# Performance work log

Hardware: AMD Instinct MI355X
Metric: run time of the kernel (lower is better)

Reference implementation:

```python
import jax, jax.numpy as jnp
import numpy as np

B, S, D_MODEL, H = 2, 2048, 1024, 16
DIMS = D_MODEL // H  # 64


def setup_inputs() -> dict:
    key = jax.random.key(0)
    ks = jax.random.split(key, 7)
    scale = 1.0 / np.sqrt(D_MODEL)
    x = jax.random.normal(ks[0], (B, S, D_MODEL), dtype=jnp.float32)
    # Stacked per-head projection params: nn.Linear(d_model, dims) per head
    Wq = jax.random.uniform(ks[1], (H, DIMS, D_MODEL), minval=-scale, maxval=scale, dtype=jnp.float32)
    Wk = jax.random.uniform(ks[2], (H, DIMS, D_MODEL), minval=-scale, maxval=scale, dtype=jnp.float32)
    Wv = jax.random.uniform(ks[3], (H, DIMS, D_MODEL), minval=-scale, maxval=scale, dtype=jnp.float32)
    bq = jax.random.uniform(ks[4], (H, DIMS), minval=-scale, maxval=scale, dtype=jnp.float32)
    bk = jax.random.uniform(ks[5], (H, DIMS), minval=-scale, maxval=scale, dtype=jnp.float32)
    bv = jax.random.uniform(ks[6], (H, DIMS), minval=-scale, maxval=scale, dtype=jnp.float32)
    return {"x": x, "Wq": Wq, "Wk": Wk, "Wv": Wv, "bq": bq, "bk": bk, "bv": bv}


def reference(x, Wq, Wk, Wv, bq, bk, bv):
    # Per-head linear projections: [B,S,D] x [H,E,D] -> [B,H,S,E]
    q = jnp.einsum('bsd,hed->bhse', x, Wq) + bq[None, :, None, :]
    k = jnp.einsum('bsd,hed->bhse', x, Wk) + bk[None, :, None, :]
    v = jnp.einsum('bsd,hed->bhse', x, Wv) + bv[None, :, None, :]
    norm = DIMS ** (-0.5)
    # (q @ k^T) * norm @ v  -- NO softmax, as in the source
    scores = jnp.einsum('bhse,bhte->bhst', q, k) * norm  # [B,H,S,S]
    out = jnp.einsum('bhst,bhte->bhse', scores, v)       # [B,H,S,E]
    # concat heads along feature dim (head order matches torch.cat)
    return out.transpose(0, 2, 1, 3).reshape(B, S, H * DIMS)
```

## Files before the change

kernel.cpp:

```cpp
#include <hip/hip_runtime.h>


typedef __attribute__((ext_vector_type(8))) __bf16 bf16x8;
typedef __attribute__((ext_vector_type(8))) short short8;
typedef __attribute__((ext_vector_type(4))) float f32x4;
typedef __attribute__((ext_vector_type(4))) unsigned short ushort4v;

#define NX  4194304
#define NW1 1048576
#define NW  3145728

__device__ __forceinline__ float bf2f(unsigned short u) {
  union { unsigned int i; float f; } v; v.i = ((unsigned int)u) << 16; return v.f;
}
__device__ __forceinline__ unsigned short f2bf(float f) {
  union { float f; unsigned int i; } v; v.f = f;
  unsigned int u = v.i;
  u += 0x7fffu + ((u >> 16) & 1u);
  return (unsigned short)(u >> 16);
}

__device__ __forceinline__ void gload_lds16(const void* g, void* l) {
  __builtin_amdgcn_global_load_lds(
      (const __attribute__((address_space(1))) void*)(unsigned long long)(g),
      (__attribute__((address_space(3))) void*)(unsigned int)(unsigned long long)(l),
      16, 0, 0);
}

__global__ __launch_bounds__(256) void convert_pack(
    const float* __restrict__ x,
    const float* __restrict__ wq, const float* __restrict__ wk,
    const float* __restrict__ wv,
    const float* __restrict__ bq, const float* __restrict__ bk,
    const float* __restrict__ bv,
    unsigned short* __restrict__ Xbf, unsigned short* __restrict__ Wcat,
    float* __restrict__ Bcat)
{
  const long long t8 = ((long long)blockIdx.x * 256 + threadIdx.x) * 8;
  const float* src;
  unsigned short* dst;
  long long off;
  if (t8 < NX) {
    src = x; dst = Xbf; off = t8;
  } else if (t8 < NX + NW) {
    const long long w = t8 - NX;
    const int z = (int)(w >> 20);
    off = w & (NW1 - 1);
    src = (z == 0) ? wq : (z == 1) ? wk : wv;
    dst = Wcat + (long long)z * NW1;
  } else if (t8 < NX + NW + 3072) {
    const long long bo = t8 - (NX + NW);
    const int z = (int)(bo >> 10);
    const long long o2 = bo & 1023;
    const float* bsrc = (z == 0) ? bq : (z == 1) ? bk : bv;
    *(f32x4*)(Bcat + z * 1024 + o2)     = *(const f32x4*)(bsrc + o2);
    *(f32x4*)(Bcat + z * 1024 + o2 + 4) = *(const f32x4*)(bsrc + o2 + 4);
    return;
  } else {
    return;
  }
  f32x4 v0 = *(const f32x4*)(src + off);
  f32x4 v1 = *(const f32x4*)(src + off + 4);
  union { short8 s; unsigned short u[8]; } o;
#pragma unroll
  for (int j = 0; j < 4; ++j) {
    o.u[j]     = f2bf(v0[j]);
    o.u[4 + j] = f2bf(v1[j]);
  }
  *(short8*)(dst + off) = o.s;
}

#define ABUF_B 16384
#define BBUF_B 12288
#define TILE_B 28672
__global__ __launch_bounds__(512, 2) void qkv_gemm(
    const unsigned short* __restrict__ Xbf,
    const unsigned short* __restrict__ Wcat,
    const float* __restrict__ Bcat,
    unsigned short* __restrict__ Qt,
    unsigned short* __restrict__ Kt,
    unsigned short* __restrict__ Vt)
{
  __shared__ unsigned char lds[4 * TILE_B];

  const int tid = threadIdx.x;
  int bid = blockIdx.x;
  bid = (bid & 7) * 32 + (bid >> 3);
  const int colBase = (bid & 15) * 192;
  const int rowBase = (bid >> 4) * 256;

  const int lane = tid & 63;
  const int wid  = tid >> 6;
  const int wr = (wid >> 2) * 128;
  const int wc = (wid & 3) * 48;
  const int lr = lane & 15;
  const int lk = lane >> 4;
  const int fofs = (lk ^ ((lr >> 1) & 3)) << 4;

  const bool isA = (tid < 256);
  const int tloc = isA ? tid : (tid - 256);

  const unsigned short* gptr[4];
  int lofs[4];
#pragma unroll
  for (int l = 0; l < 4; ++l) {
    const int unit = l * 256 + tloc;
    const int row  = unit >> 2;
    const int sc   = ((unit & 3) ^ ((row >> 1) & 3)) << 3;
    const int rowc = (!isA && row > 191) ? 0 : row;
    gptr[l] = isA ? (Xbf  + (size_t)(rowBase + rowc) * 1024 + sc)
                  : (Wcat + (size_t)(colBase + rowc) * 1024 + sc);
    lofs[l] = (isA ? 0 : ABUF_B) + unit * 16;
  }

  f32x4 acc[8][3] = {};

#define STAGE(j3)                                                    \
  { unsigned char* Sb_ = lds + ((j3) & 3) * TILE_B;                  \
    const int ko_ = (j3) * 32;                                       \
    if (isA) {                                                       \
      _Pragma("unroll") for (int l = 0; l < 4; ++l)                  \
        gload_lds16(gptr[l] + ko_, Sb_ + lofs[l]);                   \
    } else {                                                         \
      _Pragma("unroll") for (int l = 0; l < 3; ++l)                  \
        gload_lds16(gptr[l] + ko_, Sb_ + lofs[l]);                   \
    } }

#define KSTEP(j, DOSTAGE, VMA, VMB)                                       \
  { if (isA) asm volatile("s_waitcnt vmcnt(" #VMA ")" ::: "memory");      \
    else     asm volatile("s_waitcnt vmcnt(" #VMB ")" ::: "memory");      \
    asm volatile("s_barrier" ::: "memory");                               \
    const unsigned char* Ab_ = lds + ((j) & 3) * TILE_B;                  \
    const unsigned char* Bb_ = Ab_ + ABUF_B;                              \
    bf16x8 a_[8], b_[3];                                                  \
    _Pragma("unroll") for (int m = 0; m < 8; ++m)                         \
      a_[m] = *(const bf16x8*)(Ab_ + (wr + m * 16 + lr) * 64 + fofs);     \
    _Pragma("unroll") for (int n = 0; n < 3; ++n)                         \
      b_[n] = *(const bf16x8*)(Bb_ + (wc + n * 16 + lr) * 64 + fofs);     \
    if (DOSTAGE) STAGE((j) + 3);                                          \
    __builtin_amdgcn_s_setprio(1);                                        \
    _Pragma("unroll") for (int m = 0; m < 8; ++m)                         \
      _Pragma("unroll") for (int n = 0; n < 3; ++n)                       \
        acc[m][n] = __builtin_amdgcn_mfma_f32_16x16x32_bf16(              \
            a_[m], b_[n], acc[m][n], 0, 0, 0);                            \
    __builtin_amdgcn_s_setprio(0);                                        \
  }

  STAGE(0); STAGE(1); STAGE(2);

  for (int j = 0; j < 29; ++j) KSTEP(j, true, 8, 6);
  KSTEP(29, false, 8, 6);
  KSTEP(30, false, 4, 3);
  KSTEP(31, false, 0, 0);
#undef KSTEP
#undef STAGE

  const int bB = rowBase >> 11;
#pragma unroll
  for (int n = 0; n < 3; ++n) {
    const int colG = colBase + wc + n * 16 + lr;
    const float bval = Bcat[colG];
    const int zone = colG >> 10;
    unsigned short* __restrict__ T = (zone == 0) ? Qt : (zone == 1) ? Kt : Vt;
    const int hf = (colG >> 6) & 15;
    const int f  = colG & 63;
    const size_t rowOff = ((size_t)(bB * 16 + hf) * 64 + f) * 2048;
#pragma unroll
    for (int m = 0; m < 8; ++m) {
      const int t = (rowBase + wr + m * 16 + lk * 4) & 2047;
      ushort4v pk;
#pragma unroll
      for (int jj = 0; jj < 4; ++jj)
        pk[jj] = f2bf(acc[m][n][jj] + bval);
      *(ushort4v*)&T[rowOff + t] = pk;
    }
  }
}

__global__ __launch_bounds__(64) void kv_outer(
    const unsigned short* __restrict__ Kt,
    const unsigned short* __restrict__ Vt,
    float* __restrict__ Mpart)
{
  const int lane = threadIdx.x;
  const int blk = blockIdx.x;
  const int bh = blk >> 3, tc = blk & 7;
  const int lr = lane & 15, lk = lane >> 4;
  const size_t base = (size_t)bh * 64 * 2048;

  f32x4 acc[4][4] = {};
#pragma unroll
  for (int ks = 0; ks < 8; ++ks) {
    const int t0 = tc * 256 + ks * 32 + lk * 8;
    bf16x8 af[4], bf[4];
#pragma unroll
    for (int m = 0; m < 4; ++m)
      af[m] = *(const bf16x8*)&Kt[base + (size_t)(m * 16 + lr) * 2048 + t0];
#pragma unroll
    for (int n = 0; n < 4; ++n)
      bf[n] = *(const bf16x8*)&Vt[base + (size_t)(n * 16 + lr) * 2048 + t0];
#pragma unroll
    for (int m = 0; m < 4; ++m)
#pragma unroll
      for (int n = 0; n < 4; ++n)
        acc[m][n] = __builtin_amdgcn_mfma_f32_16x16x32_bf16(af[m], bf[n], acc[m][n], 0, 0, 0);
  }
  float* out = Mpart + (size_t)blk * 4096;
#pragma unroll
  for (int m = 0; m < 4; ++m)
#pragma unroll
    for (int n = 0; n < 4; ++n)
#pragma unroll
      for (int j = 0; j < 4; ++j)
        out[(m * 16 + lk * 4 + j) * 64 + n * 16 + lr] = acc[m][n][j];
}

__global__ __launch_bounds__(256) void qm_out(
    const unsigned short* __restrict__ Qt, const float* __restrict__ Mpart,
    float* __restrict__ Out)
{
  __shared__ float Ms[64 * 64];
  __shared__ float Qst[64 * 132];
  const int tid = threadIdx.x;
  const int b = blockIdx.z, h = blockIdx.y, s0 = blockIdx.x * 128;
  const int bh = b * 16 + h;

#pragma unroll
  for (int i = 0; i < 4; ++i) {
    const int off = i * 1024 + tid * 4;
    f32x4 s = {};
#pragma unroll
    for (int ch = 0; ch < 8; ++ch)
      s += *(const f32x4*)&Mpart[((size_t)bh * 8 + ch) * 4096 + off];
    s *= 0.125f;
    *(f32x4*)&Ms[off] = s;
  }
  const size_t qbase = (size_t)bh * 64 * 2048;
#pragma unroll
  for (int i = 0; i < 4; ++i) {
    const int slot = i * 256 + tid;
    const int f = slot >> 4, c = slot & 15;
    short8 q = *(const short8*)&Qt[qbase + (size_t)f * 2048 + s0 + c * 8];
#pragma unroll
    for (int j = 0; j < 8; ++j)
      Qst[f * 132 + c * 8 + j] = bf2f((unsigned short)q[j]);
  }
  __syncthreads();

  const int s = (tid >> 3) * 4;
  const int e0 = (tid & 7) * 8;
  float acc2[4][8] = {};
  for (int f = 0; f < 64; ++f) {
    f32x4 m0 = *(const f32x4*)&Ms[f * 64 + e0];
    f32x4 m1 = *(const f32x4*)&Ms[f * 64 + e0 + 4];
#pragma unroll
    for (int i = 0; i < 4; ++i) {
      const float q = Qst[f * 132 + s + i];
#pragma unroll
      for (int j = 0; j < 4; ++j) {
        acc2[i][j]     += q * m0[j];
        acc2[i][j + 4] += q * m1[j];
      }
    }
  }
  const size_t obase = ((size_t)b * 2048 + s0) * 1024 + h * 64;
#pragma unroll
  for (int i = 0; i < 4; ++i) {
    f32x4 o0 = { acc2[i][0], acc2[i][1], acc2[i][2], acc2[i][3] };
    f32x4 o1 = { acc2[i][4], acc2[i][5], acc2[i][6], acc2[i][7] };
    *(f32x4*)&Out[obase + (size_t)(s + i) * 1024 + e0]     = o0;
    *(f32x4*)&Out[obase + (size_t)(s + i) * 1024 + e0 + 4] = o1;
  }
}

extern "C" void kernel_launch(void* const* d_in, const int* in_sizes, int n_in,
                              void* d_out, int out_size, void* d_ws, size_t ws_size,
                              hipStream_t stream) {
  const float* x  = (const float*)d_in[0];
  const float* Wq = (const float*)d_in[1];
  const float* Wk = (const float*)d_in[2];
  const float* Wv = (const float*)d_in[3];
  const float* bq = (const float*)d_in[4];
  const float* bk = (const float*)d_in[5];
  const float* bv = (const float*)d_in[6];
  float* out = (float*)d_out;

  char* ws = (char*)d_ws;
  const size_t MiB = 1024ull * 1024ull;
  unsigned short* Xbf   = (unsigned short*)(ws);
  unsigned short* Wcat  = (unsigned short*)(ws + 8  * MiB);
  float*          Bcat  = (float*)         (ws + 14 * MiB);
  unsigned short* Qt    = (unsigned short*)(ws + 15 * MiB);
  unsigned short* Kt    = (unsigned short*)(ws + 23 * MiB);
  unsigned short* Vt    = (unsigned short*)(ws + 31 * MiB);
  float*          Mpart = (float*)         (ws + 39 * MiB);

  convert_pack<<<3586, 256, 0, stream>>>(x, Wq, Wk, Wv, bq, bk, bv,
                                         Xbf, Wcat, Bcat);
  qkv_gemm<<<256, 512, 0, stream>>>(Xbf, Wcat, Bcat, Qt, Kt, Vt);
  kv_outer<<<256, 64, 0, stream>>>(Kt, Vt, Mpart);
  qm_out<<<dim3(16, 16, 2), 256, 0, stream>>>(Qt, Mpart, out);
}
```

Baseline: 66.50 us.

## Replace direct global-to-LDS loads with register-staged software pipeline in QKV GEMM

The QKV projection GEMM no longer uses global_load_lds DMA into a 4-deep LDS ring. Each thread now prefetches three k-steps of tiles into registers and writes the next tile into a 3-deep LDS ring while the current one is consumed by MFMAs. The LDS footprint drops by one tile, and the explicit vmcnt waits give way to compiler-managed waits plus lgkmcnt waits. The cost is many extra VGPRs for the staging buffers, which may hurt occupancy under launch_bounds(512,2), and the added LDS write instructions.

```diff
diff --git a/kernel.cpp b/kernel.cpp
--- a/kernel.cpp
+++ b/kernel.cpp
@@ -18,13 +18,6 @@
   unsigned int u = v.i;
   u += 0x7fffu + ((u >> 16) & 1u);
   return (unsigned short)(u >> 16);
-}
-
-__device__ __forceinline__ void gload_lds16(const void* g, void* l) {
-  __builtin_amdgcn_global_load_lds(
-      (const __attribute__((address_space(1))) void*)(unsigned long long)(g),
-      (__attribute__((address_space(3))) void*)(unsigned int)(unsigned long long)(l),
-      16, 0, 0);
 }
 
 __global__ __launch_bounds__(256) void convert_pack(
@@ -71,7 +64,6 @@
 }
 
 #define ABUF_B 16384
-#define BBUF_B 12288
 #define TILE_B 28672
 __global__ __launch_bounds__(512, 2) void qkv_gemm(
     const unsigned short* __restrict__ Xbf,
@@ -81,7 +73,7 @@
     unsigned short* __restrict__ Kt,
     unsigned short* __restrict__ Vt)
 {
-  __shared__ unsigned char lds[4 * TILE_B];
+  __shared__ unsigned char lds[3 * TILE_B];
 
   const int tid = threadIdx.x;
   int bid = blockIdx.x;
@@ -98,9 +90,10 @@
   const int fofs = (lk ^ ((lr >> 1) & 3)) << 4;
 
   const bool isA = (tid < 256);
-  const int tloc = isA ? tid : (tid - 256);
-
-  const unsigned short* gptr[4];
+  const int nload = isA ? 4 : 3;
+  const int tloc = tid & 255;
+
+  const unsigned short* gp[4];
   int lofs[4];
 #pragma unroll
   for (int l = 0; l < 4; ++l) {
@@ -108,52 +101,59 @@
     const int row  = unit >> 2;
     const int sc   = ((unit & 3) ^ ((row >> 1) & 3)) << 3;
     const int rowc = (!isA && row > 191) ? 0 : row;
-    gptr[l] = isA ? (Xbf  + (size_t)(rowBase + rowc) * 1024 + sc)
-                  : (Wcat + (size_t)(colBase + rowc) * 1024 + sc);
+    gp[l]  = isA ? (Xbf  + (size_t)(rowBase + rowc) * 1024 + sc)
+                 : (Wcat + (size_t)(colBase + rowc) * 1024 + sc);
     lofs[l] = (isA ? 0 : ABUF_B) + unit * 16;
   }
 
   f32x4 acc[8][3] = {};
-
-#define STAGE(j3)                                                    \
-  { unsigned char* Sb_ = lds + ((j3) & 3) * TILE_B;                  \
-    const int ko_ = (j3) * 32;                                       \
-    if (isA) {                                                       \
-      _Pragma("unroll") for (int l = 0; l < 4; ++l)                  \
-        gload_lds16(gptr[l] + ko_, Sb_ + lofs[l]);                   \
-    } else {                                                         \
-      _Pragma("unroll") for (int l = 0; l < 3; ++l)                  \
-        gload_lds16(gptr[l] + ko_, Sb_ + lofs[l]);                   \
-    } }
-
-#define KSTEP(j, DOSTAGE, VMA, VMB)                                       \
-  { if (isA) asm volatile("s_waitcnt vmcnt(" #VMA ")" ::: "memory");      \
-    else     asm volatile("s_waitcnt vmcnt(" #VMB ")" ::: "memory");      \
-    asm volatile("s_barrier" ::: "memory");                               \
-    const unsigned char* Ab_ = lds + ((j) & 3) * TILE_B;                  \
-    const unsigned char* Bb_ = Ab_ + ABUF_B;                              \
-    bf16x8 a_[8], b_[3];                                                  \
-    _Pragma("unroll") for (int m = 0; m < 8; ++m)                         \
-      a_[m] = *(const bf16x8*)(Ab_ + (wr + m * 16 + lr) * 64 + fofs);     \
-    _Pragma("unroll") for (int n = 0; n < 3; ++n)                         \
-      b_[n] = *(const bf16x8*)(Bb_ + (wc + n * 16 + lr) * 64 + fofs);     \
-    if (DOSTAGE) STAGE((j) + 3);                                          \
-    __builtin_amdgcn_s_setprio(1);                                        \
-    _Pragma("unroll") for (int m = 0; m < 8; ++m)                         \
-      _Pragma("unroll") for (int n = 0; n < 3; ++n)                       \
-        acc[m][n] = __builtin_amdgcn_mfma_f32_16x16x32_bf16(              \
-            a_[m], b_[n], acc[m][n], 0, 0, 0);                            \
-    __builtin_amdgcn_s_setprio(0);                                        \
-  }
-
-  STAGE(0); STAGE(1); STAGE(2);
-
-  for (int j = 0; j < 29; ++j) KSTEP(j, true, 8, 6);
-  KSTEP(29, false, 8, 6);
-  KSTEP(30, false, 4, 3);
-  KSTEP(31, false, 0, 0);
-#undef KSTEP
-#undef STAGE
+  short8 stg[3][4];
+
+#pragma unroll
+  for (int s = 0; s < 3; ++s)
+#pragma unroll
+    for (int l = 0; l < 4; ++l)
+      if (l < nload) stg[s][l] = *(const short8*)(gp[l] + s * 32);
+#pragma unroll
+  for (int l = 0; l < 4; ++l)
+    if (l < nload) *(short8*)(lds + lofs[l]) = stg[0][l];
+  asm volatile("s_waitcnt lgkmcnt(0)" ::: "memory");
+
+#define ITER(J, U, U1)                                                     \
+  if ((J) < 32) {                                                          \
+    __builtin_amdgcn_s_barrier();                                          \
+    __builtin_amdgcn_sched_barrier(0);                                     \
+    const unsigned char* Ab_ = lds + (U) * TILE_B;                         \
+    const unsigned char* Bb_ = Ab_ + ABUF_B;                               \
+    bf16x8 a_[8], b_[3];                                                   \
+    _Pragma("unroll") for (int m = 0; m < 8; ++m)                          \
+      a_[m] = *(const bf16x8*)(Ab_ + (wr + m * 16 + lr) * 64 + fofs);      \
+    _Pragma("unroll") for (int n = 0; n < 3; ++n)                          \
+      b_[n] = *(const bf16x8*)(Bb_ + (wc + n * 16 + lr) * 64 + fofs);      \
+    if ((J) + 1 < 32) {                                                    \
+      unsigned char* Wb_ = lds + (U1) * TILE_B;                            \
+      _Pragma("unroll") for (int l = 0; l < 4; ++l)                        \
+        if (l < nload) *(short8*)(Wb_ + lofs[l]) = stg[U1][l];             \
+    }                                                                      \
+    if ((J) + 3 < 32) {                                                    \
+      _Pragma("unroll") for (int l = 0; l < 4; ++l)                        \
+        if (l < nload) stg[U][l] = *(const short8*)(gp[l] + ((J) + 3) * 32);\
+    }                                                                      \
+    __builtin_amdgcn_s_setprio(1);                                         \
+    _Pragma("unroll") for (int m = 0; m < 8; ++m)                          \
+      _Pragma("unroll") for (int n = 0; n < 3; ++n)                        \
+        acc[m][n] = __builtin_amdgcn_mfma_f32_16x16x32_bf16(               \
+            a_[m], b_[n], acc[m][n], 0, 0, 0);                             \
+    __builtin_amdgcn_s_setprio(0);                                         \
+    asm volatile("s_waitcnt lgkmcnt(0)" ::: "memory");                     \
+  }
+
+  for (int jb = 0; jb < 32; jb += 3) {
+    ITER(jb + 0, 0, 1);
+    ITER(jb + 1, 1, 2);
+    ITER(jb + 2, 2, 0);
+  }
+#undef ITER
 
   const int bB = rowBase >> 11;
 #pragma unroll
```

Measured after the change: 67.05 us. About the same (+0.8%).

## Restructure QKV GEMM to 256x256 tiles with BK=64 double-buffered LDS

Applied to the files above, without the earlier changes.

The QKV projection GEMM now uses 256x256 output tiles (192 blocks, one block per CU) instead of 256x192 tiles (256 blocks). Each iteration loads a 64-wide K slice into one of two 64KB LDS buffers, and staging of the next slice is interleaved between the two MFMA sub-steps. The LDS XOR swizzle is dropped. The goal is more reuse per loaded byte, fewer blocks so the grid fits in one wave on 256 CUs, and fewer barriers. The trade-offs are lower occupancy (launch bounds 1), more accumulator registers, possible LDS bank conflicts now that the swizzle is gone, and 64 idle CUs.

```diff
diff --git a/kernel.cpp b/kernel.cpp
--- a/kernel.cpp
+++ b/kernel.cpp
@@ -70,10 +70,7 @@
   *(short8*)(dst + off) = o.s;
 }
 
-#define ABUF_B 16384
-#define BBUF_B 12288
-#define TILE_B 28672
-__global__ __launch_bounds__(512, 2) void qkv_gemm(
+__global__ __launch_bounds__(512, 1) void qkv_gemm(
     const unsigned short* __restrict__ Xbf,
     const unsigned short* __restrict__ Wcat,
     const float* __restrict__ Bcat,
@@ -81,83 +78,166 @@
     unsigned short* __restrict__ Kt,
     unsigned short* __restrict__ Vt)
 {
-  __shared__ unsigned char lds[4 * TILE_B];
+  __shared__ unsigned char lds[131072];
 
   const int tid = threadIdx.x;
   int bid = blockIdx.x;
-  bid = (bid & 7) * 32 + (bid >> 3);
-  const int colBase = (bid & 15) * 192;
-  const int rowBase = (bid >> 4) * 256;
+  bid = (bid & 7) * 24 + (bid >> 3);
+  const int colBase = (bid % 12) * 256;
+  const int rowBase = (bid / 12) * 256;
 
   const int lane = tid & 63;
   const int wid  = tid >> 6;
   const int wr = (wid >> 2) * 128;
-  const int wc = (wid & 3) * 48;
+  const int wc = (wid & 3) * 64;
   const int lr = lane & 15;
   const int lk = lane >> 4;
-  const int fofs = (lk ^ ((lr >> 1) & 3)) << 4;
-
-  const bool isA = (tid < 256);
-  const int tloc = isA ? tid : (tid - 256);
-
-  const unsigned short* gptr[4];
-  int lofs[4];
-#pragma unroll
-  for (int l = 0; l < 4; ++l) {
-    const int unit = l * 256 + tloc;
-    const int row  = unit >> 2;
-    const int sc   = ((unit & 3) ^ ((row >> 1) & 3)) << 3;
-    const int rowc = (!isA && row > 191) ? 0 : row;
-    gptr[l] = isA ? (Xbf  + (size_t)(rowBase + rowc) * 1024 + sc)
-                  : (Wcat + (size_t)(colBase + rowc) * 1024 + sc);
-    lofs[l] = (isA ? 0 : ABUF_B) + unit * 16;
-  }
-
-  f32x4 acc[8][3] = {};
-
-#define STAGE(j3)                                                    \
-  { unsigned char* Sb_ = lds + ((j3) & 3) * TILE_B;                  \
-    const int ko_ = (j3) * 32;                                       \
-    if (isA) {                                                       \
-      _Pragma("unroll") for (int l = 0; l < 4; ++l)                  \
-        gload_lds16(gptr[l] + ko_, Sb_ + lofs[l]);                   \
-    } else {                                                         \
-      _Pragma("unroll") for (int l = 0; l < 3; ++l)                  \
-        gload_lds16(gptr[l] + ko_, Sb_ + lofs[l]);                   \
-    } }
-
-#define KSTEP(j, DOSTAGE, VMA, VMB)                                       \
-  { if (isA) asm volatile("s_waitcnt vmcnt(" #VMA ")" ::: "memory");      \
-    else     asm volatile("s_waitcnt vmcnt(" #VMB ")" ::: "memory");      \
-    asm volatile("s_barrier" ::: "memory");                               \
-    const unsigned char* Ab_ = lds + ((j) & 3) * TILE_B;                  \
-    const unsigned char* Bb_ = Ab_ + ABUF_B;                              \
-    bf16x8 a_[8], b_[3];                                                  \
-    _Pragma("unroll") for (int m = 0; m < 8; ++m)                         \
-      a_[m] = *(const bf16x8*)(Ab_ + (wr + m * 16 + lr) * 64 + fofs);     \
-    _Pragma("unroll") for (int n = 0; n < 3; ++n)                         \
-      b_[n] = *(const bf16x8*)(Bb_ + (wc + n * 16 + lr) * 64 + fofs);     \
-    if (DOSTAGE) STAGE((j) + 3);                                          \
-    __builtin_amdgcn_s_setprio(1);                                        \
-    _Pragma("unroll") for (int m = 0; m < 8; ++m)                         \
-      _Pragma("unroll") for (int n = 0; n < 3; ++n)                       \
-        acc[m][n] = __builtin_amdgcn_mfma_f32_16x16x32_bf16(              \
-            a_[m], b_[n], acc[m][n], 0, 0, 0);                            \
-    __builtin_amdgcn_s_setprio(0);                                        \
-  }
-
-  STAGE(0); STAGE(1); STAGE(2);
-
-  for (int j = 0; j < 29; ++j) KSTEP(j, true, 8, 6);
-  KSTEP(29, false, 8, 6);
-  KSTEP(30, false, 4, 3);
-  KSTEP(31, false, 0, 0);
-#undef KSTEP
-#undef STAGE
+
+  const size_t aoff = (size_t)(rowBase + (tid >> 2)) * 1024 + (tid & 3) * 8;
+  const size_t boff = (size_t)(colBase + (tid >> 2)) * 1024 + (tid & 3) * 8;
+  const int d1 = tid * 16, d2 = 8192 + tid * 16;
+
+#define STG(secl, gsrc)                                   \
+  { gload_lds16((gsrc),               (secl) + d1);       \
+    gload_lds16((gsrc) + 128 * 1024,  (secl) + d2); }
+
+  f32x4 acc[8][4] = {};
+
+  STG(lds + 0,     Xbf  + aoff + 0);
+  STG(lds + 32768, Wcat + boff + 0);
+  STG(lds + 16384, Xbf  + aoff + 32);
+  STG(lds + 49152, Wcat + boff + 32);
+
+  const int frA = (wr + lr) * 64 + lk * 16;
+  const int frB = (wc + lr) * 64 + lk * 16;
+
+  for (int t = 0; t < 16; ++t) {
+    const unsigned char* bufc = lds + (t & 1) * 65536;
+    unsigned char* bufn = lds + ((t + 1) & 1) * 65536;
+    const size_t kno = (size_t)(t + 1) * 64;
+    const bool st = (t < 15);
+
+    bf16x8 a0, a1, a2, a3, a4, a5, a6, a7, b0, b1;
+
+    asm volatile("s_waitcnt vmcnt(4)" ::: "memory");
+    __builtin_amdgcn_s_barrier();
+    {
+      const unsigned char* As = bufc;
+      const unsigned char* Bs = bufc + 32768;
+      a0 = *(const bf16x8*)(As + frA);
+      a1 = *(const bf16x8*)(As + frA + 1024);
+      a2 = *(const bf16x8*)(As + frA + 2048);
+      a3 = *(const bf16x8*)(As + frA + 3072);
+      a4 = *(const bf16x8*)(As + frA + 4096);
+      a5 = *(const bf16x8*)(As + frA + 5120);
+      a6 = *(const bf16x8*)(As + frA + 6144);
+      a7 = *(const bf16x8*)(As + frA + 7168);
+      b0 = *(const bf16x8*)(Bs + frB);
+      b1 = *(const bf16x8*)(Bs + frB + 1024);
+      if (st) STG(bufn + 0, Xbf + aoff + kno);
+      __builtin_amdgcn_s_setprio(1);
+      acc[0][0] = __builtin_amdgcn_mfma_f32_16x16x32_bf16(a0, b0, acc[0][0], 0, 0, 0);
+      acc[1][0] = __builtin_amdgcn_mfma_f32_16x16x32_bf16(a1, b0, acc[1][0], 0, 0, 0);
+      acc[2][0] = __builtin_amdgcn_mfma_f32_16x16x32_bf16(a2, b0, acc[2][0], 0, 0, 0);
+      acc[3][0] = __builtin_amdgcn_mfma_f32_16x16x32_bf16(a3, b0, acc[3][0], 0, 0, 0);
+      acc[4][0] = __builtin_amdgcn_mfma_f32_16x16x32_bf16(a4, b0, acc[4][0], 0, 0, 0);
+      acc[5][0] = __builtin_amdgcn_mfma_f32_16x16x32_bf16(a5, b0, acc[5][0], 0, 0, 0);
+      acc[6][0] = __builtin_amdgcn_mfma_f32_16x16x32_bf16(a6, b0, acc[6][0], 0, 0, 0);
+      acc[7][0] = __builtin_amdgcn_mfma_f32_16x16x32_bf16(a7, b0, acc[7][0], 0, 0, 0);
+      acc[0][1] = __builtin_amdgcn_mfma_f32_16x16x32_bf16(a0, b1, acc[0][1], 0, 0, 0);
+      acc[1][1] = __builtin_amdgcn_mfma_f32_16x16x32_bf16(a1, b1, acc[1][1], 0, 0, 0);
+      acc[2][1] = __builtin_amdgcn_mfma_f32_16x16x32_bf16(a2, b1, acc[2][1], 0, 0, 0);
+      acc[3][1] = __builtin_amdgcn_mfma_f32_16x16x32_bf16(a3, b1, acc[3][1], 0, 0, 0);
+      acc[4][1] = __builtin_amdgcn_mfma_f32_16x16x32_bf16(a4, b1, acc[4][1], 0, 0, 0);
+      acc[5][1] = __builtin_amdgcn_mfma_f32_16x16x32_bf16(a5, b1, acc[5][1], 0, 0, 0);
+      acc[6][1] = __builtin_amdgcn_mfma_f32_16x16x32_bf16(a6, b1, acc[6][1], 0, 0, 0);
+      acc[7][1] = __builtin_amdgcn_mfma_f32_16x16x32_bf16(a7, b1, acc[7][1], 0, 0, 0);
+      __builtin_amdgcn_s_setprio(0);
+      b0 = *(const bf16x8*)(Bs + frB + 2048);
+      b1 = *(const bf16x8*)(Bs + frB + 3072);
+      if (st) STG(bufn + 32768, Wcat + boff + kno);
+      __builtin_amdgcn_s_setprio(1);
+      acc[0][2] = __builtin_amdgcn_mfma_f32_16x16x32_bf16(a0, b0, acc[0][2], 0, 0, 0);
+      acc[1][2] = __builtin_amdgcn_mfma_f32_16x16x32_bf16(a1, b0, acc[1][2], 0, 0, 0);
+      acc[2][2] = __builtin_amdgcn_mfma_f32_16x16x32_bf16(a2, b0, acc[2][2], 0, 0, 0);
+      acc[3][2] = __builtin_amdgcn_mfma_f32_16x16x32_bf16(a3, b0, acc[3][2], 0, 0, 0);
+      acc[4][2] = __builtin_amdgcn_mfma_f32_16x16x32_bf16(a4, b0, acc[4][2], 0, 0, 0);
+      acc[5][2] = __builtin_amdgcn_mfma_f32_16x16x32_bf16(a5, b0, acc[5][2], 0, 0, 0);
+      acc[6][2] = __builtin_amdgcn_mfma_f32_16x16x32_bf16(a6, b0, acc[6][2], 0, 0, 0);
+      acc[7][2] = __builtin_amdgcn_mfma_f32_16x16x32_bf16(a7, b0, acc[7][2], 0, 0, 0);
+      acc[0][3] = __builtin_amdgcn_mfma_f32_16x16x32_bf16(a0, b1, acc[0][3], 0, 0, 0);
+      acc[1][3] = __builtin_amdgcn_mfma_f32_16x16x32_bf16(a1, b1, acc[1][3], 0, 0, 0);
+      acc[2][3] = __builtin_amdgcn_mfma_f32_16x16x32_bf16(a2, b1, acc[2][3], 0, 0, 0);
+      acc[3][3] = __builtin_amdgcn_mfma_f32_16x16x32_bf16(a3, b1, acc[3][3], 0, 0, 0);
+      acc[4][3] = __builtin_amdgcn_mfma_f32_16x16x32_bf16(a4, b1, acc[4][3], 0, 0, 0);
+      acc[5][3] = __builtin_amdgcn_mfma_f32_16x16x32_bf16(a5, b1, acc[5][3], 0, 0, 0);
+      acc[6][3] = __builtin_amdgcn_mfma_f32_16x16x32_bf16(a6, b1, acc[6][3], 0, 0, 0);
+      acc[7][3] = __builtin_amdgcn_mfma_f32_16x16x32_bf16(a7, b1, acc[7][3], 0, 0, 0);
+      __builtin_amdgcn_s_setprio(0);
+    }
+    if (t < 15) asm volatile("s_waitcnt vmcnt(4)" ::: "memory");
+    else        asm volatile("s_waitcnt vmcnt(0)" ::: "memory");
+    __builtin_amdgcn_s_barrier();
+    {
+      const unsigned char* As = bufc + 16384;
+      const unsigned char* Bs = bufc + 49152;
+      a0 = *(const bf16x8*)(As + frA);
+      a1 = *(const bf16x8*)(As + frA + 1024);
+      a2 = *(const bf16x8*)(As + frA + 2048);
+      a3 = *(const bf16x8*)(As + frA + 3072);
+      a4 = *(const bf16x8*)(As + frA + 4096);
+      a5 = *(const bf16x8*)(As + frA + 5120);
+      a6 = *(const bf16x8*)(As + frA + 6144);
+      a7 = *(const bf16x8*)(As + frA + 7168);
+      b0 = *(const bf16x8*)(Bs + frB);
+      b1 = *(const bf16x8*)(Bs + frB + 1024);
+      if (st) STG(bufn + 16384, Xbf + aoff + kno + 32);
+      __builtin_amdgcn_s_setprio(1);
+      acc[0][0] = __builtin_amdgcn_mfma_f32_16x16x32_bf16(a0, b0, acc[0][0], 0, 0, 0);
+      acc[1][0] = __builtin_amdgcn_mfma_f32_16x16x32_bf16(a1, b0, acc[1][0], 0, 0, 0);
+      acc[2][0] = __builtin_amdgcn_mfma_f32_16x16x32_bf16(a2, b0, acc[2][0], 0, 0, 0);
+      acc[3][0] = __builtin_amdgcn_mfma_f32_16x16x32_bf16(a3, b0, acc[3][0], 0, 0, 0);
+      acc[4][0] = __builtin_amdgcn_mfma_f32_16x16x32_bf16(a4, b0, acc[4][0], 0, 0, 0);
+      acc[5][0] = __builtin_amdgcn_mfma_f32_16x16x32_bf16(a5, b0, acc[5][0], 0, 0, 0);
+      acc[6][0] = __builtin_amdgcn_mfma_f32_16x16x32_bf16(a6, b0, acc[6][0], 0, 0, 0);
+      acc[7][0] = __builtin_amdgcn_mfma_f32_16x16x32_bf16(a7, b0, acc[7][0], 0, 0, 0);
+      acc[0][1] = __builtin_amdgcn_mfma_f32_16x16x32_bf16(a0, b1, acc[0][1], 0, 0, 0);
+      acc[1][1] = __builtin_amdgcn_mfma_f32_16x16x32_bf16(a1, b1, acc[1][1], 0, 0, 0);
+      acc[2][1] = __builtin_amdgcn_mfma_f32_16x16x32_bf16(a2, b1, acc[2][1], 0, 0, 0);
+      acc[3][1] = __builtin_amdgcn_mfma_f32_16x16x32_bf16(a3, b1, acc[3][1], 0, 0, 0);
+      acc[4][1] = __builtin_amdgcn_mfma_f32_16x16x32_bf16(a4, b1, acc[4][1], 0, 0, 0);
+      acc[5][1] = __builtin_amdgcn_mfma_f32_16x16x32_bf16(a5, b1, acc[5][1], 0, 0, 0);
+      acc[6][1] = __builtin_amdgcn_mfma_f32_16x16x32_bf16(a6, b1, acc[6][1], 0, 0, 0);
+      acc[7][1] = __builtin_amdgcn_mfma_f32_16x16x32_bf16(a7, b1, acc[7][1], 0, 0, 0);
+      __builtin_amdgcn_s_setprio(0);
+      b0 = *(const bf16x8*)(Bs + frB + 2048);
+      b1 = *(const bf16x8*)(Bs + frB + 3072);
+      if (st) STG(bufn + 49152, Wcat + boff + kno + 32);
+      __builtin_amdgcn_s_setprio(1);
+      acc[0][2] = __builtin_amdgcn_mfma_f32_16x16x32_bf16(a0, b0, acc[0][2], 0, 0, 0);
+      acc[1][2] = __builtin_amdgcn_mfma_f32_16x16x32_bf16(a1, b0, acc[1][2], 0, 0, 0);
+      acc[2][2] = __builtin_amdgcn_mfma_f32_16x16x32_bf16(a2, b0, acc[2][2], 0, 0, 0);
+      acc[3][2] = __builtin_amdgcn_mfma_f32_16x16x32_bf16(a3, b0, acc[3][2], 0, 0, 0);
+      acc[4][2] = __builtin_amdgcn_mfma_f32_16x16x32_bf16(a4, b0, acc[4][2], 0, 0, 0);
+      acc[5][2] = __builtin_amdgcn_mfma_f32_16x16x32_bf16(a5, b0, acc[5][2], 0, 0, 0);
+      acc[6][2] = __builtin_amdgcn_mfma_f32_16x16x32_bf16(a6, b0, acc[6][2], 0, 0, 0);
+      acc[7][2] = __builtin_amdgcn_mfma_f32_16x16x32_bf16(a7, b0, acc[7][2], 0, 0, 0);
+      acc[0][3] = __builtin_amdgcn_mfma_f32_16x16x32_bf16(a0, b1, acc[0][3], 0, 0, 0);
+      acc[1][3] = __builtin_amdgcn_mfma_f32_16x16x32_bf16(a1, b1, acc[1][3], 0, 0, 0);
+      acc[2][3] = __builtin_amdgcn_mfma_f32_16x16x32_bf16(a2, b1, acc[2][3], 0, 0, 0);
+      acc[3][3] = __builtin_amdgcn_mfma_f32_16x16x32_bf16(a3, b1, acc[3][3], 0, 0, 0);
+      acc[4][3] = __builtin_amdgcn_mfma_f32_16x16x32_bf16(a4, b1, acc[4][3], 0, 0, 0);
+      acc[5][3] = __builtin_amdgcn_mfma_f32_16x16x32_bf16(a5, b1, acc[5][3], 0, 0, 0);
+      acc[6][3] = __builtin_amdgcn_mfma_f32_16x16x32_bf16(a6, b1, acc[6][3], 0, 0, 0);
+      acc[7][3] = __builtin_amdgcn_mfma_f32_16x16x32_bf16(a7, b1, acc[7][3], 0, 0, 0);
+      __builtin_amdgcn_s_setprio(0);
+    }
+  }
+#undef STG
 
   const int bB = rowBase >> 11;
 #pragma unroll
-  for (int n = 0; n < 3; ++n) {
+  for (int n = 0; n < 4; ++n) {
     const int colG = colBase + wc + n * 16 + lr;
     const float bval = Bcat[colG];
     const int zone = colG >> 10;
@@ -167,12 +247,12 @@
     const size_t rowOff = ((size_t)(bB * 16 + hf) * 64 + f) * 2048;
 #pragma unroll
     for (int m = 0; m < 8; ++m) {
-      const int t = (rowBase + wr + m * 16 + lk * 4) & 2047;
+      const int tpos = (rowBase + wr + m * 16 + lk * 4) & 2047;
       ushort4v pk;
 #pragma unroll
       for (int jj = 0; jj < 4; ++jj)
         pk[jj] = f2bf(acc[m][n][jj] + bval);
-      *(ushort4v*)&T[rowOff + t] = pk;
+      *(ushort4v*)&T[rowOff + tpos] = pk;
     }
   }
 }
@@ -297,7 +377,7 @@
 
   convert_pack<<<3586, 256, 0, stream>>>(x, Wq, Wk, Wv, bq, bk, bv,
                                          Xbf, Wcat, Bcat);
-  qkv_gemm<<<256, 512, 0, stream>>>(Xbf, Wcat, Bcat, Qt, Kt, Vt);
+  qkv_gemm<<<192, 512, 0, stream>>>(Xbf, Wcat, Bcat, Qt, Kt, Vt);
   kv_outer<<<256, 64, 0, stream>>>(Kt, Vt, Mpart);
   qm_out<<<dim3(16, 16, 2), 256, 0, stream>>>(Qt, Mpart, out);
 }
```

Result: slower. 70.49 us (+6.0%).

## Restructure QKV GEMM pipeline to double-buffered BK=64 with split stage loads

Applied to the files above, without the earlier changes.

Replaces the 4-stage ring of BK=32 tiles in the QKV projection GEMM with two 56KB buffers, each holding a BK=64 tile split into two 32-wide halves. The next tile's loads are issued in pieces between MFMA groups, and B fragments are loaded lazily to reduce register pressure. Launch bounds drop to one block per CU because of the larger LDS footprint. The goal is fewer barriers per K unit and better overlap of global-to-LDS loads with compute, at the cost of occupancy and a shallower prefetch distance.

```diff
diff --git a/kernel.cpp b/kernel.cpp
--- a/kernel.cpp
+++ b/kernel.cpp
@@ -70,10 +70,8 @@
   *(short8*)(dst + off) = o.s;
 }
 
-#define ABUF_B 16384
-#define BBUF_B 12288
-#define TILE_B 28672
-__global__ __launch_bounds__(512, 2) void qkv_gemm(
+#define BUF_B 57344
+__global__ __launch_bounds__(512, 1) void qkv_gemm(
     const unsigned short* __restrict__ Xbf,
     const unsigned short* __restrict__ Wcat,
     const float* __restrict__ Bcat,
@@ -81,7 +79,7 @@
     unsigned short* __restrict__ Kt,
     unsigned short* __restrict__ Vt)
 {
-  __shared__ unsigned char lds[4 * TILE_B];
+  __shared__ unsigned char lds[2 * BUF_B];
 
   const int tid = threadIdx.x;
   int bid = blockIdx.x;
@@ -96,64 +94,104 @@
   const int lr = lane & 15;
   const int lk = lane >> 4;
   const int fofs = (lk ^ ((lr >> 1) & 3)) << 4;
+  const int frA = (wr + lr) * 64 + fofs;
+  const int frB = (wc + lr) * 64 + fofs;
 
   const bool isA = (tid < 256);
-  const int tloc = isA ? tid : (tid - 256);
-
-  const unsigned short* gptr[4];
-  int lofs[4];
+  const int nl = isA ? 4 : 3;
+  const int tloc = tid & 255;
+
+  const unsigned short* gp[4];
+  int dofs[4];
 #pragma unroll
   for (int l = 0; l < 4; ++l) {
-    const int unit = l * 256 + tloc;
-    const int row  = unit >> 2;
-    const int sc   = ((unit & 3) ^ ((row >> 1) & 3)) << 3;
+    const int u = l * 256 + tloc;
+    const int row = u >> 2;
     const int rowc = (!isA && row > 191) ? 0 : row;
-    gptr[l] = isA ? (Xbf  + (size_t)(rowBase + rowc) * 1024 + sc)
-                  : (Wcat + (size_t)(colBase + rowc) * 1024 + sc);
-    lofs[l] = (isA ? 0 : ABUF_B) + unit * 16;
-  }
+    const int csrc = (u & 3) ^ ((rowc >> 1) & 3);
+    gp[l] = isA ? (Xbf  + (size_t)(rowBase + rowc) * 1024 + csrc * 8)
+                : (Wcat + (size_t)(colBase + rowc) * 1024 + csrc * 8);
+    dofs[l] = u * 16;
+  }
+
+#define STGRP(secbase, kofs)                                 \
+  { _Pragma("unroll") for (int l = 0; l < 4; ++l)            \
+      if (l < nl) gload_lds16(gp[l] + (kofs), (secbase) + dofs[l]); }
 
   f32x4 acc[8][3] = {};
 
-#define STAGE(j3)                                                    \
-  { unsigned char* Sb_ = lds + ((j3) & 3) * TILE_B;                  \
-    const int ko_ = (j3) * 32;                                       \
-    if (isA) {                                                       \
-      _Pragma("unroll") for (int l = 0; l < 4; ++l)                  \
-        gload_lds16(gptr[l] + ko_, Sb_ + lofs[l]);                   \
-    } else {                                                         \
-      _Pragma("unroll") for (int l = 0; l < 3; ++l)                  \
-        gload_lds16(gptr[l] + ko_, Sb_ + lofs[l]);                   \
-    } }
-
-#define KSTEP(j, DOSTAGE, VMA, VMB)                                       \
-  { if (isA) asm volatile("s_waitcnt vmcnt(" #VMA ")" ::: "memory");      \
-    else     asm volatile("s_waitcnt vmcnt(" #VMB ")" ::: "memory");      \
-    asm volatile("s_barrier" ::: "memory");                               \
-    const unsigned char* Ab_ = lds + ((j) & 3) * TILE_B;                  \
-    const unsigned char* Bb_ = Ab_ + ABUF_B;                              \
-    bf16x8 a_[8], b_[3];                                                  \
-    _Pragma("unroll") for (int m = 0; m < 8; ++m)                         \
-      a_[m] = *(const bf16x8*)(Ab_ + (wr + m * 16 + lr) * 64 + fofs);     \
-    _Pragma("unroll") for (int n = 0; n < 3; ++n)                         \
-      b_[n] = *(const bf16x8*)(Bb_ + (wc + n * 16 + lr) * 64 + fofs);     \
-    if (DOSTAGE) STAGE((j) + 3);                                          \
-    __builtin_amdgcn_s_setprio(1);                                        \
-    _Pragma("unroll") for (int m = 0; m < 8; ++m)                         \
-      _Pragma("unroll") for (int n = 0; n < 3; ++n)                       \
-        acc[m][n] = __builtin_amdgcn_mfma_f32_16x16x32_bf16(              \
-            a_[m], b_[n], acc[m][n], 0, 0, 0);                            \
-    __builtin_amdgcn_s_setprio(0);                                        \
-  }
-
-  STAGE(0); STAGE(1); STAGE(2);
-
-  for (int j = 0; j < 29; ++j) KSTEP(j, true, 8, 6);
-  KSTEP(29, false, 8, 6);
-  KSTEP(30, false, 4, 3);
-  KSTEP(31, false, 0, 0);
-#undef KSTEP
-#undef STAGE
+  if (isA) { STGRP(lds + 0,     0); STGRP(lds + 16384, 32); }
+  else     { STGRP(lds + 32768, 0); STGRP(lds + 45056, 32); }
+
+  for (int t = 0; t < 16; ++t) {
+    const unsigned char* bufc = lds + (t & 1) * BUF_B;
+    unsigned char* bufn = lds + ((t + 1) & 1) * BUF_B;
+    const size_t kno = (size_t)(t + 1) * 64;
+    const bool st = (t < 15);
+    bf16x8 a[8], b0, b1, b2;
+
+    if (isA) asm volatile("s_waitcnt vmcnt(4)" ::: "memory");
+    else     asm volatile("s_waitcnt vmcnt(3)" ::: "memory");
+    __builtin_amdgcn_s_barrier();
+    {
+      const unsigned char* As = bufc;
+      const unsigned char* Bs = bufc + 32768;
+#pragma unroll
+      for (int m = 0; m < 8; ++m)
+        a[m] = *(const bf16x8*)(As + frA + m * 1024);
+      b0 = *(const bf16x8*)(Bs + frB);
+      b1 = *(const bf16x8*)(Bs + frB + 1024);
+      if (st && isA) STGRP(bufn + 0, kno);
+      __builtin_amdgcn_s_setprio(1);
+#pragma unroll
+      for (int m = 0; m < 8; ++m)
+        acc[m][0] = __builtin_amdgcn_mfma_f32_16x16x32_bf16(a[m], b0, acc[m][0], 0, 0, 0);
+#pragma unroll
+      for (int m = 0; m < 8; ++m)
+        acc[m][1] = __builtin_amdgcn_mfma_f32_16x16x32_bf16(a[m], b1, acc[m][1], 0, 0, 0);
+      __builtin_amdgcn_s_setprio(0);
+      b2 = *(const bf16x8*)(Bs + frB + 2048);
+      if (st && !isA) STGRP(bufn + 32768, kno);
+      __builtin_amdgcn_s_setprio(1);
+#pragma unroll
+      for (int m = 0; m < 8; ++m)
+        acc[m][2] = __builtin_amdgcn_mfma_f32_16x16x32_bf16(a[m], b2, acc[m][2], 0, 0, 0);
+      __builtin_amdgcn_s_setprio(0);
+    }
+    if (st) {
+      if (isA) asm volatile("s_waitcnt vmcnt(4)" ::: "memory");
+      else     asm volatile("s_waitcnt vmcnt(3)" ::: "memory");
+    } else {
+      asm volatile("s_waitcnt vmcnt(0)" ::: "memory");
+    }
+    __builtin_amdgcn_s_barrier();
+    {
+      const unsigned char* As = bufc + 16384;
+      const unsigned char* Bs = bufc + 45056;
+#pragma unroll
+      for (int m = 0; m < 8; ++m)
+        a[m] = *(const bf16x8*)(As + frA + m * 1024);
+      b0 = *(const bf16x8*)(Bs + frB);
+      b1 = *(const bf16x8*)(Bs + frB + 1024);
+      if (st && isA) STGRP(bufn + 16384, kno + 32);
+      __builtin_amdgcn_s_setprio(1);
+#pragma unroll
+      for (int m = 0; m < 8; ++m)
+        acc[m][0] = __builtin_amdgcn_mfma_f32_16x16x32_bf16(a[m], b0, acc[m][0], 0, 0, 0);
+#pragma unroll
+      for (int m = 0; m < 8; ++m)
+        acc[m][1] = __builtin_amdgcn_mfma_f32_16x16x32_bf16(a[m], b1, acc[m][1], 0, 0, 0);
+      __builtin_amdgcn_s_setprio(0);
+      b2 = *(const bf16x8*)(Bs + frB + 2048);
+      if (st && !isA) STGRP(bufn + 45056, kno + 32);
+      __builtin_amdgcn_s_setprio(1);
+#pragma unroll
+      for (int m = 0; m < 8; ++m)
+        acc[m][2] = __builtin_amdgcn_mfma_f32_16x16x32_bf16(a[m], b2, acc[m][2], 0, 0, 0);
+      __builtin_amdgcn_s_setprio(0);
+    }
+  }
+#undef STGRP
 
   const int bB = rowBase >> 11;
 #pragma unroll
@@ -167,12 +205,12 @@
     const size_t rowOff = ((size_t)(bB * 16 + hf) * 64 + f) * 2048;
 #pragma unroll
     for (int m = 0; m < 8; ++m) {
-      const int t = (rowBase + wr + m * 16 + lk * 4) & 2047;
+      const int tpos = (rowBase + wr + m * 16 + lk * 4) & 2047;
       ushort4v pk;
 #pragma unroll
       for (int jj = 0; jj < 4; ++jj)
         pk[jj] = f2bf(acc[m][n][jj] + bval);
-      *(ushort4v*)&T[rowOff + t] = pk;
+      *(ushort4v*)&T[rowOff + tpos] = pk;
     }
   }
 }
```

Result: no change. 66.31 us (-0.3%).
